# Optimization experiments

Hardware: AMD Instinct MI355X
Metric: run time of the kernel (lower is better)

## Reference

```python
import jax, jax.numpy as jnp
import numpy as np

IMG_H, IMG_W = 512.0, 512.0
PRED_SIZES = [(64, 64), (32, 32), (16, 16), (8, 8), (4, 4), (2, 2)]
ASPECT_RATIOS = [1.0, 2.0, 0.5, 3.0]
SCALES = [0.04, 0.1, 0.26, 0.42, 0.58, 0.74]
N_CLASSES = 21
CONF_THRESH = 0.01
IOU_THRESH = 0.45
TOP_K = 100
NMS_MAX = 200
XY_VAR, WH_VAR = 0.1, 0.2
NEG = -1e30  # stand-in for -inf that is safe under autodiff


def generate_boxes():
    # Standard SSD anchors (cx, cy, w, h), normalized to [0, 1].
    all_boxes = []
    for (fh, fw), s in zip(PRED_SIZES, SCALES):
        cx = (np.arange(fw, dtype=np.float32) + 0.5) / fw
        cy = (np.arange(fh, dtype=np.float32) + 0.5) / fh
        cxg, cyg = np.meshgrid(cx, cy)  # [fh, fw]
        for ar in ASPECT_RATIOS:
            w = s * np.sqrt(ar)
            h = s / np.sqrt(ar)
            b = np.stack([cxg, cyg, np.full_like(cxg, w), np.full_like(cxg, h)], axis=-1)
            all_boxes.append(b.reshape(-1, 4))
    return np.concatenate(all_boxes, axis=0).astype(np.float32)  # [21840, 4]


def setup_inputs() -> dict:
    key = jax.random.key(0)
    n_boxes = sum(fh * fw for fh, fw in PRED_SIZES) * len(ASPECT_RATIOS)
    y_pred = jax.random.normal(key, (32, n_boxes, N_CLASSES + 4), dtype=jnp.float32)
    box_tensor = jnp.asarray(generate_boxes())
    return {"y_pred": y_pred, "box_tensor": box_tensor}


def _decode(y_pred, box_tensor):
    # y_pred: [B, N, C+4], box_tensor: [N, 4] (cx, cy, w, h)
    logits = y_pred[..., :-4]
    class_ids = jnp.argmax(logits, axis=-1).astype(jnp.float32)  # [B, N]
    confidences = jnp.max(logits, axis=-1)                       # [B, N]
    a_cx, a_cy, a_w, a_h = box_tensor[:, 0], box_tensor[:, 1], box_tensor[:, 2], box_tensor[:, 3]
    cx = y_pred[..., -4] * XY_VAR * a_w + a_cx
    cy = y_pred[..., -3] * XY_VAR * a_h + a_cy
    w = jnp.exp(y_pred[..., -2] * WH_VAR) * a_w
    h = jnp.exp(y_pred[..., -1] * WH_VAR) * a_h
    xmin = jnp.clip(cx - 0.5 * w, 0.0, 1.0)
    ymin = jnp.clip(cy - 0.5 * h, 0.0, 1.0)
    xmax = jnp.clip(cx + 0.5 * w, 0.0, 1.0)
    ymax = jnp.clip(cy + 0.5 * h, 0.0, 1.0)
    # [B, N, 6]: class_id, confidence, xmin, ymin, xmax, ymax
    return jnp.stack([class_ids, confidences, xmin, ymin, xmax, ymax], axis=-1)


def _nms_image(preds):
    # preds: [N, 6]. Greedy NMS over confident, non-background boxes, then top-k.
    N = preds.shape[0]
    valid = (preds[:, 0] != 0.0) & (preds[:, 1] > CONF_THRESH)
    scores0 = jnp.where(valid, preds[:, 1], NEG)
    boxes = preds[:, 2:6]  # xmin, ymin, xmax, ymax
    areas = (boxes[:, 2] - boxes[:, 0]) * (boxes[:, 3] - boxes[:, 1])
    idxs = jnp.arange(N)

    def step(scores, _):
        i = jnp.argmax(scores)
        best = scores[i]
        ok = best > NEG * 0.5
        b = boxes[i]
        ix1 = jnp.maximum(b[0], boxes[:, 0])
        iy1 = jnp.maximum(b[1], boxes[:, 1])
        ix2 = jnp.minimum(b[2], boxes[:, 2])
        iy2 = jnp.minimum(b[3], boxes[:, 3])
        inter = jnp.maximum(ix2 - ix1, 0.0) * jnp.maximum(iy2 - iy1, 0.0)
        union = areas[i] + areas - inter
        iou = jnp.where(union > 0.0, inter / jnp.maximum(union, 1e-12), 0.0)
        suppress = (iou > IOU_THRESH) | (idxs == i)
        new_scores = jnp.where(ok & suppress, NEG, scores)
        row = jnp.where(ok, preds[i], 0.0)         # zero-pad like the TF pad path
        s = jnp.where(ok, best, 0.0)               # pad rows get score 0
        return new_scores, (row, s)

    _, (rows, sel_scores) = jax.lax.scan(step, scores0, None, length=NMS_MAX)
    # rows: [NMS_MAX, 6] in descending score order; top_k like the TF layer.
    _, ti = jax.lax.top_k(sel_scores, TOP_K)
    return rows[ti]  # [TOP_K, 6]


def reference(y_pred, box_tensor):
    preds = _decode(y_pred, box_tensor)          # [B, N, 6]
    return jax.vmap(_nms_image)(preds)           # [B, TOP_K, 6]
```

## Files before the change

kernel.cpp:

```cpp
#include <hip/hip_runtime.h>
#include <math.h>

typedef unsigned long long ull;
typedef unsigned int uint;

#define NBOX 21840
#define SEGSZ 512
#define NSEG 44
#define NPAD (NSEG*SEGSZ)
#define PFXS 23
#define OUTW 24
#define NWALK (NSEG*PFXS)
#define MCAP 1024
#define WIN 512
#define BATCH 32
#define NCLS 21
#define NEGV -1e30f
#define MIOU (15099494.5/33554432.0)

__device__ __forceinline__ uint key_hi(float s) {
    uint b = __float_as_uint(s);
    uint m = (uint)((int)b >> 31) | 0x80000000u;
    return ~(b ^ m);
}
__device__ __forceinline__ float key_score(uint hi) {
    uint srt = ~hi;
    uint b = (srt & 0x80000000u) ? (srt ^ 0x80000000u) : ~srt;
    return __uint_as_float(b);
}

__device__ __forceinline__ float area_of(float4 b) {
    return __fmul_rn(__fsub_rn(b.z, b.x), __fsub_rn(b.w, b.y));
}
__device__ __forceinline__ bool sup_check(float4 a, float aarea, float4 c, float carea) {
    float ix1 = fmaxf(a.x, c.x), iy1 = fmaxf(a.y, c.y);
    float ix2 = fminf(a.z, c.z), iy2 = fminf(a.w, c.w);
    float inter = __fmul_rn(fmaxf(__fsub_rn(ix2, ix1), 0.f), fmaxf(__fsub_rn(iy2, iy1), 0.f));
    float uni = __fsub_rn(__fadd_rn(aarea, carea), inter);
    return (uni > 0.f) && ((double)inter > MIOU * (double)fmaxf(uni, 1e-12f));
}

__device__ __forceinline__ ull cex_shfl(ull v, int j, bool asc, int lane) {
    ull pv = __shfl_xor(v, j);
    bool keepmin = (((lane & j) == 0) == asc);
    bool less = (v < pv);
    return (keepmin == less) ? v : pv;
}

__global__ __launch_bounds__(512) void decode_sort_kernel(
    const float* __restrict__ y_pred, const float* __restrict__ box_tensor,
    float4* __restrict__ BX, ull* __restrict__ KS, ull* __restrict__ KS2)
{
    __shared__ float st[SEGSZ * 25];
    __shared__ ull mbuf[8 * 24];
    int img = blockIdx.y, seg = blockIdx.x, tid = threadIdx.x;
    int wid = tid >> 6, lane = tid & 63;
    int b0 = seg * SEGSZ;
    int nval = NBOX - b0; nval = nval < 0 ? 0 : (nval > SEGSZ ? SEGSZ : nval);
    if (nval > 0) {
        const float* src = y_pred + ((size_t)img * NBOX + b0) * 25;
        int nf = nval * 25, nf4 = nf >> 2;
        const float4* src4 = (const float4*)src;
        float4* st4 = (float4*)st;
        for (int f = tid; f < nf4; f += 512) st4[f] = src4[f];
        for (int f = (nf4 << 2) + tid; f < nf; f += 512) st[f] = src[f];
    }
    __syncthreads();
    int i = b0 + tid;
    size_t o = (size_t)img * NPAD + i;
    ull v;
    if (tid < nval) {
        const float* yl = st + tid * 25;
        float best = yl[0]; int bi = 0;
        #pragma unroll
        for (int k = 1; k < NCLS; k++) { float x = yl[k]; if (x > best) { best = x; bi = k; } }
        float4 a = ((const float4*)box_tensor)[i];
        float t0 = yl[21], t1 = yl[22], t2 = yl[23], t3 = yl[24];
        float cx = __fadd_rn(__fmul_rn(__fmul_rn(t0, 0.1f), a.z), a.x);
        float cy = __fadd_rn(__fmul_rn(__fmul_rn(t1, 0.1f), a.w), a.y);
        float w  = __fmul_rn((float)exp((double)__fmul_rn(t2, 0.2f)), a.z);
        float h  = __fmul_rn((float)exp((double)__fmul_rn(t3, 0.2f)), a.w);
        float hw = __fmul_rn(0.5f, w), hh = __fmul_rn(0.5f, h);
        float xmin = fminf(fmaxf(__fsub_rn(cx, hw), 0.f), 1.f);
        float ymin = fminf(fmaxf(__fsub_rn(cy, hh), 0.f), 1.f);
        float xmax = fminf(fmaxf(__fadd_rn(cx, hw), 0.f), 1.f);
        float ymax = fminf(fmaxf(__fadd_rn(cy, hh), 0.f), 1.f);
        bool valid = (bi != 0) && (best > 0.01f);
        BX[o] = make_float4(xmin, ymin, xmax, ymax);
        uint hi = valid ? key_hi(best) : __float_as_uint(NEGV);
        v = ((ull)hi << 32) | ((uint)(i << 8)) | (uint)bi;
    } else {
        v = ((ull)__float_as_uint(NEGV) << 32) | ((uint)(i << 8));
    }
    KS[o] = v;

    for (int k = 2; k <= 64; k <<= 1) {
        bool asc = (k == 64) || ((lane & k) == 0);
        for (int j = k >> 1; j >= 1; j >>= 1)
            v = cex_shfl(v, j, asc, lane);
    }
    if (lane < 24) mbuf[wid * 24 + lane] = v;
    __syncthreads();

    if (wid != 0) return;

    ull m[4];
    #pragma unroll
    for (int r = 0; r < 4; r++) {
        int e = (r << 6) + lane;
        m[r] = (e < 192) ? mbuf[e] : ~0ull;
    }
    for (int k = 2; k <= 256; k <<= 1) {
        #pragma unroll
        for (int jr = 2; jr >= 1; jr >>= 1) {
            int j = jr << 6;
            if ((k >> 1) >= j) {
                #pragma unroll
                for (int r = 0; r < 4; r++) {
                    if ((r & jr) == 0) {
                        int rh = r | jr;
                        int e = (r << 6) + lane;
                        bool asc = ((e & k) == 0) || (k == 256);
                        ull a = m[r], b = m[rh];
                        if ((a > b) == asc) { m[r] = b; m[rh] = a; }
                    }
                }
            }
        }
        int j0 = (k >> 1) < 32 ? (k >> 1) : 32;
        for (int j = j0; j >= 1; j >>= 1) {
            #pragma unroll
            for (int r = 0; r < 4; r++) {
                int e = (r << 6) + lane;
                bool asc = ((e & k) == 0) || (k == 256);
                m[r] = cex_shfl(m[r], j, asc, lane);
            }
        }
    }
    if (lane < OUTW) KS2[(size_t)img * (NSEG * OUTW) + seg * OUTW + lane] = m[0];
}

__global__ __launch_bounds__(512) void nms_kernel(
    const ull* __restrict__ KS2, const ull* __restrict__ KS,
    const float4* __restrict__ BX, float* __restrict__ out)
{
    __shared__ ull klist[MCAP];
    __shared__ float4 cbox[WIN];
    __shared__ ull scol[WIN];
    __shared__ float4 accbox[100];
    __shared__ float  accarea[100];
    __shared__ ull pref[NSEG];

    int img = blockIdx.x, tid = threadIdx.x;
    int wid = tid >> 6, lane = tid & 63;
    const ull* ks2i = KS2 + (size_t)img * (NSEG * OUTW);
    const float4* BXg = BX + (size_t)img * NPAD;

    ull v[2];
    #pragma unroll
    for (int r = 0; r < 2; r++) {
        int e = (wid << 7) + (r << 6) + lane;
        v[r] = (e < NWALK) ? ks2i[(e / PFXS) * OUTW + (e % PFXS)] : ~0ull;
    }
    if (tid < NSEG) pref[tid] = ks2i[tid * OUTW + PFXS];

    for (int k = 2; k <= MCAP; k <<= 1) {
        if ((k >> 1) >= 128) {
            #pragma unroll
            for (int r = 0; r < 2; r++) klist[(wid << 7) + (r << 6) + lane] = v[r];
            for (int j = k >> 1; j >= 128; j >>= 1) {
                __syncthreads();
                int t = tid;
                int i = ((t & ~(j - 1)) << 1) | (t & (j - 1));
                int l = i | j;
                ull a = klist[i], b = klist[l];
                if ((a > b) == ((i & k) == 0)) { klist[i] = b; klist[l] = a; }
            }
            __syncthreads();
            #pragma unroll
            for (int r = 0; r < 2; r++) v[r] = klist[(wid << 7) + (r << 6) + lane];
        }
        if ((k >> 1) >= 64) {
            int e = (wid << 7) + lane;
            bool asc = ((e & k) == 0);
            ull a = v[0], b = v[1];
            if ((a > b) == asc) { v[0] = b; v[1] = a; }
        }
        int j0 = (k >> 1) < 32 ? (k >> 1) : 32;
        for (int j = j0; j >= 1; j >>= 1) {
            #pragma unroll
            for (int r = 0; r < 2; r++) {
                int e = (wid << 7) + (r << 6) + lane;
                v[r] = cex_shfl(v[r], j, (e & k) == 0, lane);
            }
        }
    }
    #pragma unroll
    for (int r = 0; r < 2; r++) klist[(wid << 7) + (r << 6) + lane] = v[r];
    __syncthreads();

    {
        int c = (wid << 6) + lane;
        ull k = klist[c];
        float4 bx = BXg[((uint)k) >> 8];
        cbox[c] = bx;
        float myar = area_of(bx);
        ull col = 0;
        #pragma unroll 4
        for (int i = 0; i < 64; i++) {
            float4 ib = cbox[(wid << 6) + i];
            bool s = (i < lane) && sup_check(ib, area_of(ib), bx, myar);
            col |= ((ull)s) << i;
        }
        scol[c] = col;
    }
    __syncthreads();

    if (tid >= 64) return;
    float* orow = out + (size_t)img * 600;
    const ull* ksg = KS + (size_t)img * NPAD;

    ull cutk = ~0ull;
    for (int s = 0; s < NSEG; s++) { ull x = pref[s]; if (x < cutk) cutk = x; }

    int A = 0, stop = 0, done = 0;
    int acc0 = 0, acc1 = 0;

    for (int base = 0; base < WIN && !stop; base += 64) {
        int c = base + lane;
        ull kk = klist[c];
        float4 bb = cbox[c];
        float ca = area_of(bb);
        ull mycol = scol[c];
        bool valid = !(kk >> 63) && (kk < cutk);
        ull vmask = __ballot(valid);
        bool alive = valid;
        for (int a = 0; a < A; a++)
            alive = alive & !sup_check(accbox[a], accarea[a], bb, ca);
        ull m = __ballot(alive);
        while (m && A < 100) {
            int i = __ffsll(m) - 1;
            if (lane == i) { accbox[A] = bb; accarea[A] = ca; }
            if (lane == (A & 63)) { if (A < 64) acc0 = base + i; else acc1 = base + i; }
            A++;
            m &= ~(1ull << i);
            m &= __ballot(!((mycol >> i) & 1ull));
        }
        if (A >= 100) { stop = 1; done = 1; }
        else if (vmask != ~0ull) {
            stop = 1;
            int fi = __ffsll(~vmask) - 1;
            ull fk = __shfl(kk, fi);
            done = (fk >= cutk) ? (int)(cutk >> 63) : 1;
        }
        __builtin_amdgcn_wave_barrier();
    }

    int accW = A;
    if (lane < accW) {
        ull k = klist[acc0]; float4 b = cbox[acc0];
        float* o = orow + lane * 6;
        o[0] = (float)((uint)k & 0xffu); o[1] = key_score((uint)(k >> 32));
        o[2] = b.x; o[3] = b.y; o[4] = b.z; o[5] = b.w;
    }
    if (64 + lane < accW) {
        ull k = klist[acc1]; float4 b = cbox[acc1];
        float* o = orow + (64 + lane) * 6;
        o[0] = (float)((uint)k & 0xffu); o[1] = key_score((uint)(k >> 32));
        o[2] = b.x; o[3] = b.y; o[4] = b.z; o[5] = b.w;
    }

    if (!stop) {
        for (int base = WIN; base < MCAP && !stop; base += 64) {
            int pos = base + lane;
            ull kk = klist[pos];
            bool valid = !(kk >> 63) && (kk < cutk);
            ull vmask = __ballot(valid);
            float4 bb = BXg[((uint)kk) >> 8];
            float ca = area_of(bb);
            bool alive = valid;
            for (int a = 0; a < A; a++)
                alive = alive & !sup_check(accbox[a], accarea[a], bb, ca);
            ull cand = __ballot(alive);
            while (cand && A < 100) {
                int i = __ffsll(cand) - 1;
                float4 ib = make_float4(__shfl(bb.x, i), __shfl(bb.y, i),
                                        __shfl(bb.z, i), __shfl(bb.w, i));
                float ia = __shfl(ca, i);
                ull row = __ballot(sup_check(ib, ia, bb, ca));
                if (lane == i) {
                    accbox[A] = bb; accarea[A] = ca;
                    float* o = orow + A * 6;
                    o[0] = (float)((uint)kk & 0xffu); o[1] = key_score((uint)(kk >> 32));
                    o[2] = bb.x; o[3] = bb.y; o[4] = bb.z; o[5] = bb.w;
                }
                A++;
                cand &= ~(1ull << i);
                cand &= ~row;
            }
            if (A >= 100) { stop = 1; done = 1; }
            else if (vmask != ~0ull) {
                stop = 1;
                int fi = __ffsll(~vmask) - 1;
                ull fk = __shfl(kk, fi);
                done = (fk >= cutk) ? (int)(cutk >> 63) : 1;
            }
            __builtin_amdgcn_wave_barrier();
        }
        if (!stop) done = (int)(cutk >> 63);
    }

    if (!done && A < 100) {
        ull nextk = cutk;
        while (A < 100) {
            ull best = ~0ull;
            for (int e = lane; e < NPAD; e += 64) {
                ull kk2 = ksg[e];
                if (kk2 >= nextk && kk2 < best) best = kk2;
            }
            #pragma unroll
            for (int off = 32; off; off >>= 1) {
                ull oo = __shfl_xor(best, off);
                if (oo < best) best = oo;
            }
            if (best >> 63) break;
            uint bhi = (uint)(best >> 32), blo = (uint)best;
            float4 cb = BXg[blo >> 8];
            float ca2 = area_of(cb);
            bool sup2 = false;
            #pragma unroll
            for (int t = 0; t < 2; t++) {
                int slot = lane + 64 * t;
                if (slot < A && sup_check(accbox[slot], accarea[slot], cb, ca2)) sup2 = true;
            }
            if (__ballot(sup2) == 0ull) {
                if (lane == 0) {
                    accbox[A] = cb; accarea[A] = ca2;
                    float* o = orow + A * 6;
                    o[0] = (float)(blo & 0xffu); o[1] = key_score(bhi);
                    o[2] = cb.x; o[3] = cb.y; o[4] = cb.z; o[5] = cb.w;
                }
                A++;
            }
            nextk = best + 1;
            __builtin_amdgcn_wave_barrier();
        }
    }

    for (int r = lane; r < (100 - A) * 6; r += 64) orow[A * 6 + r] = 0.f;
}

extern "C" void kernel_launch(void* const* d_in, const int* in_sizes, int n_in,
                              void* d_out, int out_size, void* d_ws, size_t ws_size,
                              hipStream_t stream)
{
    const float* y_pred     = (const float*)d_in[0];
    const float* box_tensor = (const float*)d_in[1];
    float* out = (float*)d_out;

    size_t stride = (size_t)BATCH * NPAD;
    ull*    KS  = (ull*)d_ws;
    float4* BX  = (float4*)(KS + stride);
    ull*    KS2 = (ull*)(BX + stride);

    decode_sort_kernel<<<dim3(NSEG, BATCH), 512, 0, stream>>>(y_pred, box_tensor, BX, KS, KS2);
    nms_kernel<<<BATCH, 512, 0, stream>>>(KS2, KS, BX, out);
}
```

Before: 139.6 us.

## Fuse decode-sort and NMS into one kernel with last-block-per-image handoff

```diff
diff --git a/kernel.cpp b/kernel.cpp
--- a/kernel.cpp
+++ b/kernel.cpp
@@ -40,6 +40,18 @@
     return (uni > 0.f) && ((double)inter > MIOU * (double)fmaxf(uni, 1e-12f));
 }
 
+__device__ __forceinline__ float4 decode_box(float t0, float t1, float t2, float t3, float4 a) {
+    float cx = __fadd_rn(__fmul_rn(__fmul_rn(t0, 0.1f), a.z), a.x);
+    float cy = __fadd_rn(__fmul_rn(__fmul_rn(t1, 0.1f), a.w), a.y);
+    float w  = __fmul_rn((float)exp((double)__fmul_rn(t2, 0.2f)), a.z);
+    float h  = __fmul_rn((float)exp((double)__fmul_rn(t3, 0.2f)), a.w);
+    float hw = __fmul_rn(0.5f, w), hh = __fmul_rn(0.5f, h);
+    return make_float4(fminf(fmaxf(__fsub_rn(cx, hw), 0.f), 1.f),
+                       fminf(fmaxf(__fsub_rn(cy, hh), 0.f), 1.f),
+                       fminf(fmaxf(__fadd_rn(cx, hw), 0.f), 1.f),
+                       fminf(fmaxf(__fadd_rn(cy, hh), 0.f), 1.f));
+}
+
 __device__ __forceinline__ ull cex_shfl(ull v, int j, bool asc, int lane) {
     ull pv = __shfl_xor(v, j);
     bool keepmin = (((lane & j) == 0) == asc);
@@ -47,172 +59,182 @@
     return (keepmin == less) ? v : pv;
 }
 
-__global__ __launch_bounds__(512) void decode_sort_kernel(
+__global__ __launch_bounds__(512, 6) void fused_kernel(
     const float* __restrict__ y_pred, const float* __restrict__ box_tensor,
-    float4* __restrict__ BX, ull* __restrict__ KS, ull* __restrict__ KS2)
+    ull* __restrict__ KS, ull* __restrict__ K2, float4* __restrict__ SBX,
+    int* __restrict__ ctr, float* __restrict__ out)
 {
-    __shared__ float st[SEGSZ * 25];
-    __shared__ ull mbuf[8 * 24];
+    __shared__ union {
+        struct { float st[SEGSZ * 25]; ull mbuf[8 * 24]; } d;
+        struct { ull klist[MCAP]; float4 cbox[WIN]; ull scol[WIN];
+                 float4 accbox[100]; float accarea[100]; ull pref[NSEG]; } n;
+    } sh;
+    __shared__ int flag;
+
     int img = blockIdx.y, seg = blockIdx.x, tid = threadIdx.x;
     int wid = tid >> 6, lane = tid & 63;
     int b0 = seg * SEGSZ;
+
     int nval = NBOX - b0; nval = nval < 0 ? 0 : (nval > SEGSZ ? SEGSZ : nval);
     if (nval > 0) {
         const float* src = y_pred + ((size_t)img * NBOX + b0) * 25;
         int nf = nval * 25, nf4 = nf >> 2;
         const float4* src4 = (const float4*)src;
-        float4* st4 = (float4*)st;
+        float4* st4 = (float4*)sh.d.st;
         for (int f = tid; f < nf4; f += 512) st4[f] = src4[f];
-        for (int f = (nf4 << 2) + tid; f < nf; f += 512) st[f] = src[f];
+        for (int f = (nf4 << 2) + tid; f < nf; f += 512) sh.d.st[f] = src[f];
     }
     __syncthreads();
     int i = b0 + tid;
-    size_t o = (size_t)img * NPAD + i;
     ull v;
     if (tid < nval) {
-        const float* yl = st + tid * 25;
+        const float* yl = sh.d.st + tid * 25;
         float best = yl[0]; int bi = 0;
         #pragma unroll
         for (int k = 1; k < NCLS; k++) { float x = yl[k]; if (x > best) { best = x; bi = k; } }
         float4 a = ((const float4*)box_tensor)[i];
-        float t0 = yl[21], t1 = yl[22], t2 = yl[23], t3 = yl[24];
-        float cx = __fadd_rn(__fmul_rn(__fmul_rn(t0, 0.1f), a.z), a.x);
-        float cy = __fadd_rn(__fmul_rn(__fmul_rn(t1, 0.1f), a.w), a.y);
-        float w  = __fmul_rn((float)exp((double)__fmul_rn(t2, 0.2f)), a.z);
-        float h  = __fmul_rn((float)exp((double)__fmul_rn(t3, 0.2f)), a.w);
-        float hw = __fmul_rn(0.5f, w), hh = __fmul_rn(0.5f, h);
-        float xmin = fminf(fmaxf(__fsub_rn(cx, hw), 0.f), 1.f);
-        float ymin = fminf(fmaxf(__fsub_rn(cy, hh), 0.f), 1.f);
-        float xmax = fminf(fmaxf(__fadd_rn(cx, hw), 0.f), 1.f);
-        float ymax = fminf(fmaxf(__fadd_rn(cy, hh), 0.f), 1.f);
         bool valid = (bi != 0) && (best > 0.01f);
-        BX[o] = make_float4(xmin, ymin, xmax, ymax);
         uint hi = valid ? key_hi(best) : __float_as_uint(NEGV);
-        v = ((ull)hi << 32) | ((uint)(i << 8)) | (uint)bi;
+        v = ((ull)hi << 32) | ((uint)(i << 16)) | (uint)bi;
     } else {
-        v = ((ull)__float_as_uint(NEGV) << 32) | ((uint)(i << 8));
-    }
-    KS[o] = v;
+        v = ((ull)__float_as_uint(NEGV) << 32) | ((uint)(i << 16));
+    }
+    KS[(size_t)img * NPAD + b0 + tid] = v;
 
     for (int k = 2; k <= 64; k <<= 1) {
         bool asc = (k == 64) || ((lane & k) == 0);
         for (int j = k >> 1; j >= 1; j >>= 1)
             v = cex_shfl(v, j, asc, lane);
     }
-    if (lane < 24) mbuf[wid * 24 + lane] = v;
-    __syncthreads();
-
-    if (wid != 0) return;
-
-    ull m[4];
-    #pragma unroll
-    for (int r = 0; r < 4; r++) {
-        int e = (r << 6) + lane;
-        m[r] = (e < 192) ? mbuf[e] : ~0ull;
-    }
-    for (int k = 2; k <= 256; k <<= 1) {
+    if (lane < 24) sh.d.mbuf[wid * 24 + lane] = v;
+    __syncthreads();
+
+    if (wid == 0) {
+        ull m[4];
         #pragma unroll
-        for (int jr = 2; jr >= 1; jr >>= 1) {
-            int j = jr << 6;
-            if ((k >> 1) >= j) {
+        for (int r = 0; r < 4; r++) {
+            int e = (r << 6) + lane;
+            m[r] = (e < 192) ? sh.d.mbuf[e] : ~0ull;
+        }
+        for (int k = 2; k <= 256; k <<= 1) {
+            #pragma unroll
+            for (int jr = 2; jr >= 1; jr >>= 1) {
+                int j = jr << 6;
+                if ((k >> 1) >= j) {
+                    #pragma unroll
+                    for (int r = 0; r < 4; r++) {
+                        if ((r & jr) == 0) {
+                            int rh = r | jr;
+                            int e = (r << 6) + lane;
+                            bool asc = ((e & k) == 0) || (k == 256);
+                            ull a = m[r], b = m[rh];
+                            if ((a > b) == asc) { m[r] = b; m[rh] = a; }
+                        }
+                    }
+                }
+            }
+            int j0 = (k >> 1) < 32 ? (k >> 1) : 32;
+            for (int j = j0; j >= 1; j >>= 1) {
                 #pragma unroll
                 for (int r = 0; r < 4; r++) {
-                    if ((r & jr) == 0) {
-                        int rh = r | jr;
-                        int e = (r << 6) + lane;
-                        bool asc = ((e & k) == 0) || (k == 256);
-                        ull a = m[r], b = m[rh];
-                        if ((a > b) == asc) { m[r] = b; m[rh] = a; }
-                    }
+                    int e = (r << 6) + lane;
+                    bool asc = ((e & k) == 0) || (k == 256);
+                    m[r] = cex_shfl(m[r], j, asc, lane);
                 }
             }
         }
-        int j0 = (k >> 1) < 32 ? (k >> 1) : 32;
-        for (int j = j0; j >= 1; j >>= 1) {
-            #pragma unroll
-            for (int r = 0; r < 4; r++) {
-                int e = (r << 6) + lane;
-                bool asc = ((e & k) == 0) || (k == 256);
-                m[r] = cex_shfl(m[r], j, asc, lane);
-            }
-        }
-    }
-    if (lane < OUTW) KS2[(size_t)img * (NSEG * OUTW) + seg * OUTW + lane] = m[0];
-}
-
-__global__ __launch_bounds__(512) void nms_kernel(
-    const ull* __restrict__ KS2, const ull* __restrict__ KS,
-    const float4* __restrict__ BX, float* __restrict__ out)
-{
-    __shared__ ull klist[MCAP];
-    __shared__ float4 cbox[WIN];
-    __shared__ ull scol[WIN];
-    __shared__ float4 accbox[100];
-    __shared__ float  accarea[100];
-    __shared__ ull pref[NSEG];
-
-    int img = blockIdx.x, tid = threadIdx.x;
-    int wid = tid >> 6, lane = tid & 63;
-    const ull* ks2i = KS2 + (size_t)img * (NSEG * OUTW);
-    const float4* BXg = BX + (size_t)img * NPAD;
-
-    ull v[2];
+        ull m0 = m[0];
+        size_t krow = (size_t)img * (NSEG * OUTW) + seg * OUTW;
+        if (lane < PFXS) {
+            int slot = seg * PFXS + lane;
+            K2[krow + lane] = m0 | ((ull)(slot << 5));
+            float4 bx = make_float4(9.f, 9.f, 9.f, 9.f);
+            if (!(m0 >> 63)) {
+                uint idx = (uint)((m0 >> 16) & 0x7FFFull);
+                int loc = (int)idx - b0;
+                const float* yl = sh.d.st + loc * 25;
+                float4 a = ((const float4*)box_tensor)[idx];
+                bx = decode_box(yl[21], yl[22], yl[23], yl[24], a);
+            }
+            SBX[(size_t)img * NWALK + slot] = bx;
+        } else if (lane == PFXS) {
+            K2[krow + PFXS] = m0;
+        }
+    }
+
+    __threadfence();
+    __syncthreads();
+    if (tid == 0) {
+        int old = atomicAdd(&ctr[img], 1);
+        flag = (old == NSEG - 1);
+    }
+    __syncthreads();
+    if (!flag) return;
+    __threadfence();
+
+    const ull* k2i = K2 + (size_t)img * (NSEG * OUTW);
+    const float4* SBXg = SBX + (size_t)img * NWALK;
+
+    ull v2[2];
     #pragma unroll
     for (int r = 0; r < 2; r++) {
         int e = (wid << 7) + (r << 6) + lane;
-        v[r] = (e < NWALK) ? ks2i[(e / PFXS) * OUTW + (e % PFXS)] : ~0ull;
-    }
-    if (tid < NSEG) pref[tid] = ks2i[tid * OUTW + PFXS];
+        v2[r] = (e < NWALK) ? k2i[(e / PFXS) * OUTW + (e % PFXS)] : ~0ull;
+    }
+    ull prefv = (tid < NSEG) ? k2i[tid * OUTW + PFXS] : ~0ull;
+    __syncthreads();
+    if (tid < NSEG) sh.n.pref[tid] = prefv;
 
     for (int k = 2; k <= MCAP; k <<= 1) {
         if ((k >> 1) >= 128) {
             #pragma unroll
-            for (int r = 0; r < 2; r++) klist[(wid << 7) + (r << 6) + lane] = v[r];
+            for (int r = 0; r < 2; r++) sh.n.klist[(wid << 7) + (r << 6) + lane] = v2[r];
             for (int j = k >> 1; j >= 128; j >>= 1) {
                 __syncthreads();
                 int t = tid;
-                int i = ((t & ~(j - 1)) << 1) | (t & (j - 1));
-                int l = i | j;
-                ull a = klist[i], b = klist[l];
-                if ((a > b) == ((i & k) == 0)) { klist[i] = b; klist[l] = a; }
+                int ii = ((t & ~(j - 1)) << 1) | (t & (j - 1));
+                int l = ii | j;
+                ull a = sh.n.klist[ii], b = sh.n.klist[l];
+                if ((a > b) == ((ii & k) == 0)) { sh.n.klist[ii] = b; sh.n.klist[l] = a; }
             }
             __syncthreads();
             #pragma unroll
-            for (int r = 0; r < 2; r++) v[r] = klist[(wid << 7) + (r << 6) + lane];
+            for (int r = 0; r < 2; r++) v2[r] = sh.n.klist[(wid << 7) + (r << 6) + lane];
         }
         if ((k >> 1) >= 64) {
             int e = (wid << 7) + lane;
             bool asc = ((e & k) == 0);
-            ull a = v[0], b = v[1];
-            if ((a > b) == asc) { v[0] = b; v[1] = a; }
+            ull a = v2[0], b = v2[1];
+            if ((a > b) == asc) { v2[0] = b; v2[1] = a; }
         }
         int j0 = (k >> 1) < 32 ? (k >> 1) : 32;
         for (int j = j0; j >= 1; j >>= 1) {
             #pragma unroll
             for (int r = 0; r < 2; r++) {
                 int e = (wid << 7) + (r << 6) + lane;
-                v[r] = cex_shfl(v[r], j, (e & k) == 0, lane);
+                v2[r] = cex_shfl(v2[r], j, (e & k) == 0, lane);
             }
         }
     }
     #pragma unroll
-    for (int r = 0; r < 2; r++) klist[(wid << 7) + (r << 6) + lane] = v[r];
+    for (int r = 0; r < 2; r++) sh.n.klist[(wid << 7) + (r << 6) + lane] = v2[r];
     __syncthreads();
 
     {
         int c = (wid << 6) + lane;
-        ull k = klist[c];
-        float4 bx = BXg[((uint)k) >> 8];
-        cbox[c] = bx;
+        ull k = sh.n.klist[c];
+        float4 bx = make_float4(9.f, 9.f, 9.f, 9.f);
+        if (!(k >> 63)) bx = SBXg[(uint)((k >> 5) & 0x7FFull)];
+        sh.n.cbox[c] = bx;
         float myar = area_of(bx);
         ull col = 0;
         #pragma unroll 4
-        for (int i = 0; i < 64; i++) {
-            float4 ib = cbox[(wid << 6) + i];
-            bool s = (i < lane) && sup_check(ib, area_of(ib), bx, myar);
-            col |= ((ull)s) << i;
-        }
-        scol[c] = col;
+        for (int q = 0; q < 64; q++) {
+            float4 ib = sh.n.cbox[(wid << 6) + q];
+            bool s = (q < lane) && sup_check(ib, area_of(ib), bx, myar);
+            col |= ((ull)s) << q;
+        }
+        sh.n.scol[c] = col;
     }
     __syncthreads();
 
@@ -221,30 +243,30 @@
     const ull* ksg = KS + (size_t)img * NPAD;
 
     ull cutk = ~0ull;
-    for (int s = 0; s < NSEG; s++) { ull x = pref[s]; if (x < cutk) cutk = x; }
+    for (int s = 0; s < NSEG; s++) { ull x = sh.n.pref[s]; if (x < cutk) cutk = x; }
 
     int A = 0, stop = 0, done = 0;
     int acc0 = 0, acc1 = 0;
 
     for (int base = 0; base < WIN && !stop; base += 64) {
         int c = base + lane;
-        ull kk = klist[c];
-        float4 bb = cbox[c];
+        ull kk = sh.n.klist[c];
+        float4 bb = sh.n.cbox[c];
         float ca = area_of(bb);
-        ull mycol = scol[c];
+        ull mycol = sh.n.scol[c];
         bool valid = !(kk >> 63) && (kk < cutk);
         ull vmask = __ballot(valid);
         bool alive = valid;
         for (int a = 0; a < A; a++)
-            alive = alive & !sup_check(accbox[a], accarea[a], bb, ca);
+            alive = alive & !sup_check(sh.n.accbox[a], sh.n.accarea[a], bb, ca);
         ull m = __ballot(alive);
         while (m && A < 100) {
-            int i = __ffsll(m) - 1;
-            if (lane == i) { accbox[A] = bb; accarea[A] = ca; }
-            if (lane == (A & 63)) { if (A < 64) acc0 = base + i; else acc1 = base + i; }
+            int q = __ffsll(m) - 1;
+            if (lane == q) { sh.n.accbox[A] = bb; sh.n.accarea[A] = ca; }
+            if (lane == (A & 63)) { if (A < 64) acc0 = base + q; else acc1 = base + q; }
             A++;
-            m &= ~(1ull << i);
-            m &= __ballot(!((mycol >> i) & 1ull));
+            m &= ~(1ull << q);
+            m &= __ballot(!((mycol >> q) & 1ull));
         }
         if (A >= 100) { stop = 1; done = 1; }
         else if (vmask != ~0ull) {
@@ -258,44 +280,45 @@
 
     int accW = A;
     if (lane < accW) {
-        ull k = klist[acc0]; float4 b = cbox[acc0];
+        ull k = sh.n.klist[acc0]; float4 b = sh.n.cbox[acc0];
         float* o = orow + lane * 6;
-        o[0] = (float)((uint)k & 0xffu); o[1] = key_score((uint)(k >> 32));
+        o[0] = (float)((uint)k & 0x1Fu); o[1] = key_score((uint)(k >> 32));
         o[2] = b.x; o[3] = b.y; o[4] = b.z; o[5] = b.w;
     }
     if (64 + lane < accW) {
-        ull k = klist[acc1]; float4 b = cbox[acc1];
+        ull k = sh.n.klist[acc1]; float4 b = sh.n.cbox[acc1];
         float* o = orow + (64 + lane) * 6;
-        o[0] = (float)((uint)k & 0xffu); o[1] = key_score((uint)(k >> 32));
+        o[0] = (float)((uint)k & 0x1Fu); o[1] = key_score((uint)(k >> 32));
         o[2] = b.x; o[3] = b.y; o[4] = b.z; o[5] = b.w;
     }
 
     if (!stop) {
         for (int base = WIN; base < MCAP && !stop; base += 64) {
             int pos = base + lane;
-            ull kk = klist[pos];
+            ull kk = sh.n.klist[pos];
             bool valid = !(kk >> 63) && (kk < cutk);
             ull vmask = __ballot(valid);
-            float4 bb = BXg[((uint)kk) >> 8];
+            float4 bb = make_float4(9.f, 9.f, 9.f, 9.f);
+            if (!(kk >> 63)) bb = SBXg[(uint)((kk >> 5) & 0x7FFull)];
             float ca = area_of(bb);
             bool alive = valid;
             for (int a = 0; a < A; a++)
-                alive = alive & !sup_check(accbox[a], accarea[a], bb, ca);
+                alive = alive & !sup_check(sh.n.accbox[a], sh.n.accarea[a], bb, ca);
             ull cand = __ballot(alive);
             while (cand && A < 100) {
-                int i = __ffsll(cand) - 1;
-                float4 ib = make_float4(__shfl(bb.x, i), __shfl(bb.y, i),
-                                        __shfl(bb.z, i), __shfl(bb.w, i));
-                float ia = __shfl(ca, i);
+                int q = __ffsll(cand) - 1;
+                float4 ib = make_float4(__shfl(bb.x, q), __shfl(bb.y, q),
+                                        __shfl(bb.z, q), __shfl(bb.w, q));
+                float ia = __shfl(ca, q);
                 ull row = __ballot(sup_check(ib, ia, bb, ca));
-                if (lane == i) {
-                    accbox[A] = bb; accarea[A] = ca;
+                if (lane == q) {
+                    sh.n.accbox[A] = bb; sh.n.accarea[A] = ca;
                     float* o = orow + A * 6;
-                    o[0] = (float)((uint)kk & 0xffu); o[1] = key_score((uint)(kk >> 32));
+                    o[0] = (float)((uint)kk & 0x1Fu); o[1] = key_score((uint)(kk >> 32));
                     o[2] = bb.x; o[3] = bb.y; o[4] = bb.z; o[5] = bb.w;
                 }
                 A++;
-                cand &= ~(1ull << i);
+                cand &= ~(1ull << q);
                 cand &= ~row;
             }
             if (A >= 100) { stop = 1; done = 1; }
@@ -324,20 +347,23 @@
                 if (oo < best) best = oo;
             }
             if (best >> 63) break;
-            uint bhi = (uint)(best >> 32), blo = (uint)best;
-            float4 cb = BXg[blo >> 8];
+            uint bhi = (uint)(best >> 32);
+            uint idx = (uint)((best >> 16) & 0x7FFFull);
+            float4 a = ((const float4*)box_tensor)[idx];
+            const float* yp = y_pred + ((size_t)img * NBOX + idx) * 25;
+            float4 cb = decode_box(yp[21], yp[22], yp[23], yp[24], a);
             float ca2 = area_of(cb);
             bool sup2 = false;
             #pragma unroll
             for (int t = 0; t < 2; t++) {
                 int slot = lane + 64 * t;
-                if (slot < A && sup_check(accbox[slot], accarea[slot], cb, ca2)) sup2 = true;
+                if (slot < A && sup_check(sh.n.accbox[slot], sh.n.accarea[slot], cb, ca2)) sup2 = true;
             }
             if (__ballot(sup2) == 0ull) {
                 if (lane == 0) {
-                    accbox[A] = cb; accarea[A] = ca2;
+                    sh.n.accbox[A] = cb; sh.n.accarea[A] = ca2;
                     float* o = orow + A * 6;
-                    o[0] = (float)(blo & 0xffu); o[1] = key_score(bhi);
+                    o[0] = (float)((uint)best & 0x1Fu); o[1] = key_score(bhi);
                     o[2] = cb.x; o[3] = cb.y; o[4] = cb.z; o[5] = cb.w;
                 }
                 A++;
@@ -358,11 +384,12 @@
     const float* box_tensor = (const float*)d_in[1];
     float* out = (float*)d_out;
 
-    size_t stride = (size_t)BATCH * NPAD;
-    ull*    KS  = (ull*)d_ws;
-    float4* BX  = (float4*)(KS + stride);
-    ull*    KS2 = (ull*)(BX + stride);
-
-    decode_sort_kernel<<<dim3(NSEG, BATCH), 512, 0, stream>>>(y_pred, box_tensor, BX, KS, KS2);
-    nms_kernel<<<BATCH, 512, 0, stream>>>(KS2, KS, BX, out);
-}
+    int* ctr = (int*)d_ws;
+    ull* KS  = (ull*)((char*)d_ws + 256);
+    ull* K2  = KS + (size_t)BATCH * NPAD;
+    float4* SBX = (float4*)(K2 + (size_t)BATCH * NSEG * OUTW);
+
+    hipMemsetAsync(ctr, 0, 256, stream);
+    fused_kernel<<<dim3(NSEG, BATCH), 512, 0, stream>>>(
+        y_pred, box_tensor, KS, K2, SBX, ctr, out);
+}
```

After: 426.0 us. +205.1%, slower.
